# Performance work log

Hardware: AMD Instinct MI355X
Metric: run time of the kernel (lower is better)

Reference implementation:

```python
import jax, jax.numpy as jnp
import numpy as np

B, S, HID = 1, 2048, 4096
NH, NKV, D = 32, 8, 128          # query heads, kv heads, head_dim
GROUPS = NH // NKV               # GQA repeat factor = 4
WINDOW = 1024                    # sliding-window size
ROPE_BASE = 10000.0


def setup_inputs() -> dict:
    key = jax.random.key(0)
    k = jax.random.split(key, 5)
    hidden_states = jax.random.normal(k[0], (B, S, HID), jnp.float32)
    Wq = jax.random.normal(k[1], (HID, HID), jnp.float32) * 0.02
    Wk = jax.random.normal(k[2], (NKV * D, HID), jnp.float32) * 0.02
    Wv = jax.random.normal(k[3], (NKV * D, HID), jnp.float32) * 0.02
    Wo = jax.random.normal(k[4], (HID, HID), jnp.float32) * 0.02
    position_ids = jnp.arange(S, dtype=jnp.int64 if jax.config.jax_enable_x64 else jnp.int32)[None, :]
    # Sliding-window causal additive mask [B,1,S,S]: key j visible to query i iff i-WINDOW < j <= i
    i = jnp.arange(S)
    visible = (i[None, :] <= i[:, None]) & (i[:, None] - i[None, :] < WINDOW)
    neg = jnp.finfo(jnp.float32).min
    attention_mask = jnp.where(visible, 0.0, neg)[None, None, :, :].astype(jnp.float32)
    return {"hidden_states": hidden_states, "attention_mask": attention_mask,
            "position_ids": position_ids, "Wq": Wq, "Wk": Wk, "Wv": Wv, "Wo": Wo}


def _rotate_half(x):
    x1, x2 = x[..., : D // 2], x[..., D // 2:]
    return jnp.concatenate((-x2, x1), axis=-1)


def _rope_cos_sin(position_ids, dtype):
    # inv_freq over even dims; gather-by-position_ids == direct indexing
    inv_freq = 1.0 / (ROPE_BASE ** (jnp.arange(0, D, 2, dtype=jnp.float32) / D))  # [D/2]
    freqs = position_ids.astype(jnp.float32)[..., None] * inv_freq                # [B,S,D/2]
    emb = jnp.concatenate((freqs, freqs), axis=-1)                                # [B,S,D]
    cos = jnp.cos(emb)[:, None, :, :].astype(dtype)                               # [B,1,S,D]
    sin = jnp.sin(emb)[:, None, :, :].astype(dtype)
    return cos, sin


def reference(hidden_states, attention_mask, position_ids, Wq, Wk, Wv, Wo):
    bsz, q_len, _ = hidden_states.shape
    # projections (nn.Linear: y = x @ W.T)
    q = (hidden_states @ Wq.T).reshape(bsz, q_len, NH, D).transpose(0, 2, 1, 3)    # [B,NH,S,D]
    k = (hidden_states @ Wk.T).reshape(bsz, q_len, NKV, D).transpose(0, 2, 1, 3)   # [B,NKV,S,D]
    v = (hidden_states @ Wv.T).reshape(bsz, q_len, NKV, D).transpose(0, 2, 1, 3)
    cos, sin = _rope_cos_sin(position_ids, q.dtype)
    q = q * cos + _rotate_half(q) * sin
    k = k * cos + _rotate_half(k) * sin
    # GQA repeat_kv (repeat_interleave along head dim)
    k = jnp.repeat(k, GROUPS, axis=1)                                              # [B,NH,S,D]
    v = jnp.repeat(v, GROUPS, axis=1)
    scores = jnp.einsum('bhqd,bhkd->bhqk', q, k) / np.sqrt(D)                       # [B,NH,S,S]
    scores = scores + attention_mask
    scores = jnp.maximum(scores, jnp.finfo(scores.dtype).min)
    probs = jax.nn.softmax(scores.astype(jnp.float32), axis=-1).astype(q.dtype)
    out = jnp.einsum('bhqk,bhkd->bhqd', probs, v)                                   # [B,NH,S,D]
    out = out.transpose(0, 2, 1, 3).reshape(bsz, q_len, HID)
    return out @ Wo.T
```

## Files before the change

kernel.cpp:

```cpp
#include <hip/hip_runtime.h>

#define S_LEN 2048
#define HID   4096
#define NH    32
#define NKV   8
#define DH    128
#define KVD   (NKV*DH)
#define WIN   1024
#define NTOT  6144

typedef __bf16 bf16_t;
typedef __bf16 bfrag  __attribute__((ext_vector_type(8)));
typedef __bf16 bf4    __attribute__((ext_vector_type(4)));
typedef float  ffrag  __attribute__((ext_vector_type(4)));
typedef float  facc   __attribute__((ext_vector_type(16)));

__global__ __launch_bounds__(256) void f32_to_bf16_kernel(const float* __restrict__ src,
                                                          bf16_t* __restrict__ dst, int n4) {
  int i = blockIdx.x * 256 + threadIdx.x;
  if (i < n4) {
    ffrag v = *(const ffrag*)(src + (size_t)i * 4);
    bf4 o;
    o[0] = (bf16_t)v[0]; o[1] = (bf16_t)v[1]; o[2] = (bf16_t)v[2]; o[3] = (bf16_t)v[3];
    *(bf4*)(dst + (size_t)i * 4) = o;
  }
}

__global__ __launch_bounds__(256) void cvt4_kernel(const float* __restrict__ h,
    const float* __restrict__ Wq, const float* __restrict__ Wk, const float* __restrict__ Wv,
    bf16_t* __restrict__ hB, bf16_t* __restrict__ WqB,
    bf16_t* __restrict__ WkB, bf16_t* __restrict__ WvB) {
  int i = blockIdx.x * 256 + threadIdx.x;
  const int N0 = S_LEN * HID / 4;
  const int N1 = N0 + HID * HID / 4;
  const int N2 = N1 + KVD * HID / 4;
  const float* s; bf16_t* d; int off;
  if (i < N0)      { s = h;  d = hB;  off = i; }
  else if (i < N1) { s = Wq; d = WqB; off = i - N0; }
  else if (i < N2) { s = Wk; d = WkB; off = i - N1; }
  else             { s = Wv; d = WvB; off = i - N2; }
  ffrag v = *(const ffrag*)(s + (size_t)off * 4);
  bf4 o;
  o[0] = (bf16_t)v[0]; o[1] = (bf16_t)v[1]; o[2] = (bf16_t)v[2]; o[3] = (bf16_t)v[3];
  *(bf4*)(d + (size_t)off * 4) = o;
}


__device__ __forceinline__ void load_lds16(const bf16_t* g, bf16_t* l) {
  __builtin_amdgcn_global_load_lds((__attribute__((address_space(1))) void*)g,
                                   (__attribute__((address_space(3))) void*)l,
                                   16, 0, 0);
}

#define BARW() asm volatile("s_barrier" ::: "memory")
#define WAITV(n) asm volatile("s_waitcnt vmcnt(" #n ")" ::: "memory")
#define LGKM0() do { asm volatile("s_waitcnt lgkmcnt(0)" ::: "memory"); \
                     __builtin_amdgcn_sched_barrier(0); } while (0)

template <int BN, int OUT_MODE>
__device__ __forceinline__ void gemm_body(const bf16_t* __restrict__ A,
                                          const bf16_t* __restrict__ B,
                                          void* __restrict__ Cv,
                                          int row0, int col0,
                                          int N, bf16_t* lds) {
  constexpr int K     = 4096;
  constexpr int NT    = K / 64;
  constexpr int NB    = BN / 64;
  constexpr int WCOL  = BN / 2;
  constexpr int BSW   = BN / 32;
  constexpr int ABUFE = 128 * 64;
  constexpr int BBUFE = BN * 64;

  bf16_t* As0 = lds;
  bf16_t* Bs0 = lds + 2 * ABUFE;

  const int tid  = threadIdx.x;
  const int wave = tid >> 6;
  const int lane = tid & 63;
  const int wm = wave >> 1, wn = wave & 1;
  const int l31 = lane & 31, hi = lane >> 5, l7 = lane & 7;

  const int rsub = tid >> 3;
  const int sg   = (tid & 7) ^ (rsub & 7);
  const bf16_t* Ag = A + (size_t)(row0 + rsub) * K + sg * 8;
  const bf16_t* Bg = B + (size_t)(col0 + rsub) * K + sg * 8;
  const int wbase = wave * 512;

  int pgk[4];
#pragma unroll
  for (int ks = 0; ks < 4; ++ks) pgk[ks] = ((ks * 2 + hi) ^ l7) * 8;
  const int aoff = (wm * 64 + l31) * 64;
  const int boff = (wn * WCOL + l31) * 64;

  facc acc[2][NB];
#pragma unroll
  for (int mt = 0; mt < 2; ++mt)
#pragma unroll
    for (int nt = 0; nt < NB; ++nt)
#pragma unroll
      for (int j = 0; j < 16; ++j) acc[mt][nt][j] = 0.f;

  auto STAGE = [&](int t, int s) {
    const int ko = t * 64;
    bf16_t* as = As0 + s * ABUFE + wbase;
    bf16_t* bs = Bs0 + s * BBUFE + wbase;
#pragma unroll
    for (int i = 0; i < 4; ++i)
      load_lds16(Ag + (size_t)(i * 32) * K + ko, as + i * 2048);
#pragma unroll
    for (int i = 0; i < BSW; ++i)
      load_lds16(Bg + (size_t)(i * 32) * K + ko, bs + i * 2048);
  };

  STAGE(0, 0); STAGE(1, 1);
  if constexpr (BN == 192) { WAITV(10); } else { WAITV(8); }
  BARW();

  for (int t = 0; t < NT; ++t) {
    const int s = t & 1;
    const bf16_t* Asl = As0 + s * ABUFE;
    const bf16_t* Bsl = Bs0 + s * BBUFE;

#pragma unroll
    for (int ks = 0; ks < 4; ++ks) {
      bfrag av0 = *(const bfrag*)(Asl + aoff + pgk[ks]);
      bfrag av1 = *(const bfrag*)(Asl + aoff + 2048 + pgk[ks]);
      bfrag bv[NB];
#pragma unroll
      for (int nt = 0; nt < NB; ++nt)
        bv[nt] = *(const bfrag*)(Bsl + boff + nt * 2048 + pgk[ks]);
      __builtin_amdgcn_s_setprio(1);
#pragma unroll
      for (int nt = 0; nt < NB; ++nt)
        acc[0][nt] = __builtin_amdgcn_mfma_f32_32x32x16_bf16(av0, bv[nt], acc[0][nt], 0, 0, 0);
#pragma unroll
      for (int nt = 0; nt < NB; ++nt)
        acc[1][nt] = __builtin_amdgcn_mfma_f32_32x32x16_bf16(av1, bv[nt], acc[1][nt], 0, 0, 0);
      __builtin_amdgcn_s_setprio(0);
    }

    LGKM0();
    BARW();
    if (t + 2 < NT) STAGE(t + 2, s);
    if (t + 1 < NT) {
      if (t + 2 < NT) { if constexpr (BN == 192) { WAITV(10); } else { WAITV(8); } }
      else            { WAITV(0); }
      BARW();
    }
  }

  const int orow = row0 + wm * 64 + 4 * hi;
  const int ocol = col0 + wn * WCOL + l31;
#pragma unroll
  for (int mt = 0; mt < 2; ++mt)
#pragma unroll
    for (int nt = 0; nt < NB; ++nt)
#pragma unroll
      for (int j = 0; j < 16; ++j) {
        int r = orow + mt * 32 + (j & 3) + 8 * (j >> 2);
        size_t idx = (size_t)r * N + (ocol + nt * 32);
        if (OUT_MODE == 1) ((bf16_t*)Cv)[idx] = (bf16_t)acc[mt][nt][j];
        else               ((float*)Cv)[idx]  = acc[mt][nt][j];
      }
}

__global__ __launch_bounds__(256, 2) void gemm_qkv_kernel(const bf16_t* __restrict__ hB,
                                                          const bf16_t* __restrict__ Wqkv,
                                                          bf16_t* __restrict__ C) {
  __shared__ __align__(16) bf16_t lds[2 * 128 * 64 + 2 * 192 * 64];
  const int raw  = blockIdx.x;
  const int xcd  = raw & 7;
  const int slot = raw >> 3;
  const int bx   = xcd * 4 + (slot & 3);
  const int by   = slot >> 2;
  gemm_body<192, 1>(hB, Wqkv, C, by * 128, bx * 192, NTOT, lds);
}

__global__ __launch_bounds__(256, 2) void gemm_out_kernel(const bf16_t* __restrict__ A,
                                                          const bf16_t* __restrict__ B,
                                                          float* __restrict__ out) {
  __shared__ __align__(16) bf16_t lds[2 * 128 * 64 + 2 * 128 * 64];
  const int raw  = blockIdx.x;
  const int xcd  = raw & 7;
  const int slot = raw >> 3;
  const int bx   = xcd * 4 + (slot & 3);
  const int by   = slot >> 2;
  gemm_body<128, 0>(A, B, out, by * 128, bx * 128, HID, lds);
}

__global__ __launch_bounds__(256) void ropecvt_kernel(const bf16_t* __restrict__ Cqkv,
                                                      bf16_t* __restrict__ Qb,
                                                      bf16_t* __restrict__ Kb,
                                                      bf16_t* __restrict__ Vb) {
  int idx = blockIdx.x * 256 + threadIdx.x;
  int g  = idx & 7;
  int t  = idx >> 3;
  int hh = t % 48;
  int s  = t / 48;
  const bf16_t* r0 = Cqkv + (size_t)s * NTOT + hh * 128;
  bfrag a0 = *(const bfrag*)&r0[g * 8];
  bfrag a1 = *(const bfrag*)&r0[g * 8 + 64];
  bf16_t* p;
  bool rope;
  if (hh < NH)           { p = Qb + (size_t)s * HID + hh * DH;        rope = true; }
  else if (hh < NH+NKV)  { p = Kb + (size_t)s * KVD + (hh - NH) * DH; rope = true; }
  else                   { p = Vb + (size_t)s * KVD + (hh - 40) * DH; rope = false; }
  bfrag o1, o2;
#pragma unroll
  for (int j = 0; j < 8; ++j) {
    float x1 = (float)a0[j];
    float x2 = (float)a1[j];
    if (rope) {
      int d = g * 8 + j;
      float inv = exp2f((float)d * (-13.287712379549449f / 64.f));
      float ang = (float)s * inv;
      float sn = sinf(ang), cs = cosf(ang);
      o1[j] = (bf16_t)(x1 * cs - x2 * sn);
      o2[j] = (bf16_t)(x2 * cs + x1 * sn);
    } else {
      o1[j] = (bf16_t)x1;
      o2[j] = (bf16_t)x2;
    }
  }
  *(bfrag*)&p[g * 8]      = o1;
  *(bfrag*)&p[g * 8 + 64] = o2;
}

#define KS_STRIDE 136
#define VT_STRIDE 72
#define PS_STRIDE 72

__global__ __launch_bounds__(256, 3) void attn_kernel(const bf16_t* __restrict__ Q,
                                                      const bf16_t* __restrict__ Kc,
                                                      const bf16_t* __restrict__ Vc,
                                                      bf16_t* __restrict__ AO) {
  const int qt   = 31 - blockIdx.x;
  const int h    = blockIdx.y;
  const int kvh  = h >> 2;
  const int q0   = qt * 64;
  const int tid  = threadIdx.x;
  const int wq   = tid >> 6;
  const int lane = tid & 63;
  const int n    = lane & 15;
  const int quad = lane >> 4;
  const float scale = 0.08838834764831845f;

  __shared__ __align__(16) bf16_t Ks[64 * KS_STRIDE];
  __shared__ __align__(16) bf16_t VT[128 * VT_STRIDE];
  __shared__ __align__(16) bf16_t Ps[4][16 * PS_STRIDE];

  bfrag aq[4];
#pragma unroll
  for (int kc = 0; kc < 4; ++kc) {
    bfrag t = *(const bfrag*)&Q[(size_t)(q0 + wq * 16 + n) * HID + h * DH + kc * 32 + quad * 8];
#pragma unroll
    for (int e = 0; e < 8; ++e) t[e] = (bf16_t)((float)t[e] * scale);
    aq[kc] = t;
  }

  ffrag acc[8];
#pragma unroll
  for (int dt = 0; dt < 8; ++dt) { acc[dt][0] = 0.f; acc[dt][1] = 0.f; acc[dt][2] = 0.f; acc[dt][3] = 0.f; }
  float lrow[4] = {0.f, 0.f, 0.f, 0.f};

  const int ktlo = (q0 >= WIN) ? ((q0 - (WIN - 1)) >> 6) : 0;
  const int kthi = (q0 + 63) >> 6;

  const int kg = tid & 15;
  const int dg = tid >> 4;

  bfrag pk[4], pv[4];
  {
    const int k0 = ktlo * 64;
#pragma unroll
    for (int i = 0; i < 4; ++i) {
      int pos = i * 256 + tid;
      pk[i] = *(const bfrag*)&Kc[(size_t)(k0 + (pos >> 4)) * KVD + kvh * DH + (pos & 15) * 8];
    }
#pragma unroll
    for (int j = 0; j < 4; ++j)
      pv[j] = *(const bfrag*)&Vc[(size_t)(k0 + j * 16 + kg) * KVD + kvh * DH + dg * 8];
  }

  for (int kt = ktlo; kt <= kthi; ++kt) {
    const int k0 = kt * 64;
    __syncthreads();
#pragma unroll
    for (int i = 0; i < 4; ++i) {
      int pos = i * 256 + tid;
      *(bfrag*)&Ks[(pos >> 4) * KS_STRIDE + (pos & 15) * 8] = pk[i];
    }
#pragma unroll
    for (int i = 0; i < 8; ++i) {
      bf4 pkk;
      pkk[0] = pv[0][i]; pkk[1] = pv[1][i]; pkk[2] = pv[2][i]; pkk[3] = pv[3][i];
      *(bf4*)&VT[(dg * 8 + i) * VT_STRIDE + kg * 4] = pkk;
    }
    __syncthreads();
    if (kt < kthi) {
      const int k1 = k0 + 64;
#pragma unroll
      for (int i = 0; i < 4; ++i) {
        int pos = i * 256 + tid;
        pk[i] = *(const bfrag*)&Kc[(size_t)(k1 + (pos >> 4)) * KVD + kvh * DH + (pos & 15) * 8];
      }
#pragma unroll
      for (int j = 0; j < 4; ++j)
        pv[j] = *(const bfrag*)&Vc[(size_t)(k1 + j * 16 + kg) * KVD + kvh * DH + dg * 8];
    }

    ffrag s[4];
#pragma unroll
    for (int nt = 0; nt < 4; ++nt) { s[nt][0] = 0.f; s[nt][1] = 0.f; s[nt][2] = 0.f; s[nt][3] = 0.f; }
#pragma unroll
    for (int kc = 0; kc < 4; ++kc) {
      bfrag bk[4];
#pragma unroll
      for (int nt = 0; nt < 4; ++nt)
        bk[nt] = *(const bfrag*)&Ks[(nt * 16 + n) * KS_STRIDE + kc * 32 + quad * 8];
      __builtin_amdgcn_s_setprio(1);
#pragma unroll
      for (int nt = 0; nt < 4; ++nt)
        s[nt] = __builtin_amdgcn_mfma_f32_16x16x32_bf16(aq[kc], bk[nt], s[nt], 0, 0, 0);
      __builtin_amdgcn_s_setprio(0);
    }

    const bool full = (k0 + 63 <= q0) && (q0 + 63 - k0 < WIN);
    if (!full) {
#pragma unroll
      for (int nt = 0; nt < 4; ++nt)
#pragma unroll
        for (int r = 0; r < 4; ++r) {
          int q = q0 + wq * 16 + quad * 4 + r;
          int k = k0 + nt * 16 + n;
          bool vis = (k <= q) && ((q - k) < WIN);
          if (!vis) s[nt][r] = -1e30f;
        }
    }

#pragma unroll
    for (int r = 0; r < 4; ++r) {
      bf4 pkk;
      float ps0 = __expf(s[0][r]);
      float ps1 = __expf(s[1][r]);
      float ps2 = __expf(s[2][r]);
      float ps3 = __expf(s[3][r]);
      lrow[r] += (ps0 + ps1) + (ps2 + ps3);
      pkk[0] = (bf16_t)ps0; pkk[1] = (bf16_t)ps1; pkk[2] = (bf16_t)ps2; pkk[3] = (bf16_t)ps3;
      *(bf4*)&Ps[wq][(quad * 4 + r) * PS_STRIDE + n * 4] = pkk;
    }

#pragma unroll
    for (int kc = 0; kc < 2; ++kc) {
      bfrag ap = *(const bfrag*)&Ps[wq][n * PS_STRIDE + kc * 32 + quad * 8];
#pragma unroll
      for (int dt = 0; dt < 8; dt += 4) {
        bfrag bv0 = *(const bfrag*)&VT[((dt + 0) * 16 + n) * VT_STRIDE + kc * 32 + quad * 8];
        bfrag bv1 = *(const bfrag*)&VT[((dt + 1) * 16 + n) * VT_STRIDE + kc * 32 + quad * 8];
        bfrag bv2 = *(const bfrag*)&VT[((dt + 2) * 16 + n) * VT_STRIDE + kc * 32 + quad * 8];
        bfrag bv3 = *(const bfrag*)&VT[((dt + 3) * 16 + n) * VT_STRIDE + kc * 32 + quad * 8];
        __builtin_amdgcn_s_setprio(1);
        acc[dt + 0] = __builtin_amdgcn_mfma_f32_16x16x32_bf16(ap, bv0, acc[dt + 0], 0, 0, 0);
        acc[dt + 1] = __builtin_amdgcn_mfma_f32_16x16x32_bf16(ap, bv1, acc[dt + 1], 0, 0, 0);
        acc[dt + 2] = __builtin_amdgcn_mfma_f32_16x16x32_bf16(ap, bv2, acc[dt + 2], 0, 0, 0);
        acc[dt + 3] = __builtin_amdgcn_mfma_f32_16x16x32_bf16(ap, bv3, acc[dt + 3], 0, 0, 0);
        __builtin_amdgcn_s_setprio(0);
      }
    }
  }

#pragma unroll
  for (int off = 1; off < 16; off <<= 1)
#pragma unroll
    for (int r = 0; r < 4; ++r) lrow[r] += __shfl_xor(lrow[r], off);
  float inv[4];
#pragma unroll
  for (int r = 0; r < 4; ++r) inv[r] = 1.f / lrow[r];
#pragma unroll
  for (int dt = 0; dt < 8; ++dt)
#pragma unroll
    for (int r = 0; r < 4; ++r)
      AO[(size_t)(q0 + wq * 16 + quad * 4 + r) * HID + h * DH + dt * 16 + n] =
          (bf16_t)(acc[dt][r] * inv[r]);
}

extern "C" void kernel_launch(void* const* d_in, const int* in_sizes, int n_in,
                              void* d_out, int out_size, void* d_ws, size_t ws_size,
                              hipStream_t stream) {
  const float* h  = (const float*)d_in[0];
  const float* Wq = (const float*)d_in[3];
  const float* Wk = (const float*)d_in[4];
  const float* Wv = (const float*)d_in[5];
  const float* Wo = (const float*)d_in[6];
  float* out = (float*)d_out;

  char* ws = (char*)d_ws;
  const size_t MB = (size_t)1 << 20;
  bf16_t* hB    = (bf16_t*)(ws + 0 * MB);
  bf16_t* Qb    = (bf16_t*)(ws + 0 * MB);
  bf16_t* WqB   = (bf16_t*)(ws + 16 * MB);
  bf16_t* WkB   = (bf16_t*)(ws + 48 * MB);
  bf16_t* WvB   = (bf16_t*)(ws + 56 * MB);
  bf16_t* Cqkv  = (bf16_t*)(ws + 64 * MB);
  bf16_t* WoB   = (bf16_t*)(ws + 64 * MB);
  bf16_t* AOb   = (bf16_t*)(ws + 96 * MB);
  bf16_t* Kb    = (bf16_t*)(ws + 112 * MB);
  bf16_t* Vb    = (bf16_t*)(ws + 116 * MB);

  cvt4_kernel<<<(S_LEN * HID + HID * HID + 2 * KVD * HID) / 4 / 256, 256, 0, stream>>>(
      h, Wq, Wk, Wv, hB, WqB, WkB, WvB);

  gemm_qkv_kernel<<<512, 256, 0, stream>>>(hB, WqB, Cqkv);

  ropecvt_kernel<<<(S_LEN * 48 * 8) / 256, 256, 0, stream>>>(Cqkv, Qb, Kb, Vb);

  f32_to_bf16_kernel<<<(HID * HID / 4 + 255) / 256, 256, 0, stream>>>(Wo, WoB, HID * HID / 4);

  attn_kernel<<<dim3(32, NH), 256, 0, stream>>>(Qb, Kb, Vb, AOb);

  gemm_out_kernel<<<512, 256, 0, stream>>>(AOb, WoB, out);
}
```

Baseline: 458.5 us.

## Use 512-thread 16x16x32 MFMA GEMM for QKV and precompute RoPE table

```diff
diff --git a/kernel.cpp b/kernel.cpp
--- a/kernel.cpp
+++ b/kernel.cpp
@@ -45,6 +45,13 @@
   *(bf4*)(d + (size_t)off * 4) = o;
 }
 
+__global__ __launch_bounds__(256) void rope_table_kernel(float2* __restrict__ tab) {
+  int i = blockIdx.x * 256 + threadIdx.x;
+  int s = i >> 6, d = i & 63;
+  float inv = exp2f((float)d * (-13.287712379549449f / 64.f));
+  float ang = (float)s * inv;
+  tab[i] = make_float2(cosf(ang), sinf(ang));
+}
 
 __device__ __forceinline__ void load_lds16(const bf16_t* g, bf16_t* l) {
   __builtin_amdgcn_global_load_lds((__attribute__((address_space(1))) void*)g,
@@ -57,12 +64,136 @@
 #define LGKM0() do { asm volatile("s_waitcnt lgkmcnt(0)" ::: "memory"); \
                      __builtin_amdgcn_sched_barrier(0); } while (0)
 
+template <int BNR, int OUT_MODE>
+__device__ __forceinline__ void gemm16_body(const bf16_t* __restrict__ A,
+                                            const bf16_t* __restrict__ B,
+                                            void* __restrict__ Cv,
+                                            int N, bf16_t* lds) {
+  constexpr int K     = 4096;
+  constexpr int NT    = K / 64;
+  constexpr int NTF   = BNR / 64;
+  constexpr int WC    = BNR / 4;
+  constexpr int ABUFE = 128 * 64;
+  constexpr int BBUFE = BNR * 64;
+
+  bf16_t* As0 = lds;
+  bf16_t* Bs0 = lds + 2 * ABUFE;
+
+  const int raw  = blockIdx.x;
+  const int xcd  = raw & 7;
+  const int slot = raw >> 3;
+  const int bx   = xcd * 4 + (slot & 3);
+  const int by   = slot >> 2;
+  const int row0 = by * 128;
+  const int col0 = bx * BNR;
+
+  const int tid  = threadIdx.x;
+  const int wave = tid >> 6;
+  const int lane = tid & 63;
+  const int wr = wave >> 2, wc = wave & 3;
+  const int n = lane & 15, qd = lane >> 4;
+
+  const int rsub = tid >> 3;
+  const int sg   = (tid & 7) ^ (rsub & 7);
+  const bf16_t* Ag = A + (size_t)(row0 + rsub) * K + sg * 8;
+  const bf16_t* Bg = B + (size_t)(col0 + rsub) * K + sg * 8;
+  const int wbase = wave * 512;
+
+  const int pg0 = ( qd      ^ (n & 7)) * 8;
+  const int pg1 = ((4 | qd) ^ (n & 7)) * 8;
+  const int abase = (wr * 64 + n) * 64;
+  const int bbase = (wc * WC + n) * 64;
+
+  ffrag acc[4][NTF];
+#pragma unroll
+  for (int mt = 0; mt < 4; ++mt)
+#pragma unroll
+    for (int nt = 0; nt < NTF; ++nt) {
+      acc[mt][nt][0] = 0.f; acc[mt][nt][1] = 0.f; acc[mt][nt][2] = 0.f; acc[mt][nt][3] = 0.f;
+    }
+
+  auto STAGE = [&](int t, int s) {
+    const int ko = t * 64;
+    bf16_t* as = As0 + s * ABUFE + wbase;
+    bf16_t* bs = Bs0 + s * BBUFE + wbase;
+    load_lds16(Ag + ko, as);
+    load_lds16(Ag + (size_t)64 * K + ko, as + 4096);
+    load_lds16(Bg + ko, bs);
+    load_lds16(Bg + (size_t)64 * K + ko, bs + 4096);
+    if constexpr (BNR == 192) load_lds16(Bg + (size_t)128 * K + ko, bs + 8192);
+  };
+
+  STAGE(0, 0); STAGE(1, 1);
+  if constexpr (BNR == 192) { WAITV(5); } else { WAITV(4); }
+  BARW();
+
+  for (int t = 0; t < NT; ++t) {
+    const int s = t & 1;
+    const bf16_t* Asl = As0 + s * ABUFE;
+    const bf16_t* Bsl = Bs0 + s * BBUFE;
+    bfrag av[4], bv[NTF];
+
+#pragma unroll
+    for (int mt = 0; mt < 4; ++mt) av[mt] = *(const bfrag*)(Asl + abase + mt * 1024 + pg0);
+#pragma unroll
+    for (int nt = 0; nt < NTF; ++nt) bv[nt] = *(const bfrag*)(Bsl + bbase + nt * 1024 + pg0);
+    __builtin_amdgcn_s_setprio(1);
+#pragma unroll
+    for (int mt = 0; mt < 4; ++mt)
+#pragma unroll
+      for (int nt = 0; nt < NTF; ++nt)
+        acc[mt][nt] = __builtin_amdgcn_mfma_f32_16x16x32_bf16(av[mt], bv[nt], acc[mt][nt], 0, 0, 0);
+    __builtin_amdgcn_s_setprio(0);
+
+#pragma unroll
+    for (int mt = 0; mt < 4; ++mt) av[mt] = *(const bfrag*)(Asl + abase + mt * 1024 + pg1);
+#pragma unroll
+    for (int nt = 0; nt < NTF; ++nt) bv[nt] = *(const bfrag*)(Bsl + bbase + nt * 1024 + pg1);
+    __builtin_amdgcn_s_setprio(1);
+#pragma unroll
+    for (int mt = 0; mt < 4; ++mt)
+#pragma unroll
+      for (int nt = 0; nt < NTF; ++nt)
+        acc[mt][nt] = __builtin_amdgcn_mfma_f32_16x16x32_bf16(av[mt], bv[nt], acc[mt][nt], 0, 0, 0);
+    __builtin_amdgcn_s_setprio(0);
+
+    LGKM0();
+    BARW();
+    if (t + 2 < NT) STAGE(t + 2, s);
+    if (t + 1 < NT) {
+      if (t + 2 < NT) { if constexpr (BNR == 192) { WAITV(5); } else { WAITV(4); } }
+      else            { WAITV(0); }
+      BARW();
+    }
+  }
+
+  const int orow = row0 + wr * 64 + qd * 4;
+  const int ocol = col0 + wc * WC + n;
+#pragma unroll
+  for (int mt = 0; mt < 4; ++mt)
+#pragma unroll
+    for (int nt = 0; nt < NTF; ++nt)
+#pragma unroll
+      for (int r = 0; r < 4; ++r) {
+        size_t idx = (size_t)(orow + mt * 16 + r) * N + (ocol + nt * 16);
+        if (OUT_MODE == 1) ((bf16_t*)Cv)[idx] = (bf16_t)acc[mt][nt][r];
+        else               ((float*)Cv)[idx]  = acc[mt][nt][r];
+      }
+}
+
+__global__ __launch_bounds__(512, 4) void gemm_qkv_kernel(const bf16_t* __restrict__ hB,
+                                                          const bf16_t* __restrict__ Wqkv,
+                                                          bf16_t* __restrict__ C) {
+  __shared__ __align__(16) bf16_t lds[2 * 128 * 64 + 2 * 192 * 64];
+  gemm16_body<192, 1>(hB, Wqkv, C, NTOT, lds);
+}
+
 template <int BN, int OUT_MODE>
-__device__ __forceinline__ void gemm_body(const bf16_t* __restrict__ A,
-                                          const bf16_t* __restrict__ B,
-                                          void* __restrict__ Cv,
-                                          int row0, int col0,
-                                          int N, bf16_t* lds) {
+__device__ __forceinline__ void gemm32_body(const bf16_t* __restrict__ A,
+                                            const bf16_t* __restrict__ B,
+                                            void* __restrict__ Cv,
+                                            int row0, int col0,
+                                            int N, bf16_t* lds) {
   constexpr int K     = 4096;
   constexpr int NT    = K / 64;
   constexpr int NB    = BN / 64;
@@ -113,7 +244,7 @@
   };
 
   STAGE(0, 0); STAGE(1, 1);
-  if constexpr (BN == 192) { WAITV(10); } else { WAITV(8); }
+  WAITV(8);
   BARW();
 
   for (int t = 0; t < NT; ++t) {
@@ -143,7 +274,7 @@
     BARW();
     if (t + 2 < NT) STAGE(t + 2, s);
     if (t + 1 < NT) {
-      if (t + 2 < NT) { if constexpr (BN == 192) { WAITV(10); } else { WAITV(8); } }
+      if (t + 2 < NT) { WAITV(8); }
       else            { WAITV(0); }
       BARW();
     }
@@ -162,18 +293,6 @@
         if (OUT_MODE == 1) ((bf16_t*)Cv)[idx] = (bf16_t)acc[mt][nt][j];
         else               ((float*)Cv)[idx]  = acc[mt][nt][j];
       }
-}
-
-__global__ __launch_bounds__(256, 2) void gemm_qkv_kernel(const bf16_t* __restrict__ hB,
-                                                          const bf16_t* __restrict__ Wqkv,
-                                                          bf16_t* __restrict__ C) {
-  __shared__ __align__(16) bf16_t lds[2 * 128 * 64 + 2 * 192 * 64];
-  const int raw  = blockIdx.x;
-  const int xcd  = raw & 7;
-  const int slot = raw >> 3;
-  const int bx   = xcd * 4 + (slot & 3);
-  const int by   = slot >> 2;
-  gemm_body<192, 1>(hB, Wqkv, C, by * 128, bx * 192, NTOT, lds);
 }
 
 __global__ __launch_bounds__(256, 2) void gemm_out_kernel(const bf16_t* __restrict__ A,
@@ -185,10 +304,11 @@
   const int slot = raw >> 3;
   const int bx   = xcd * 4 + (slot & 3);
   const int by   = slot >> 2;
-  gemm_body<128, 0>(A, B, out, by * 128, bx * 128, HID, lds);
+  gemm32_body<128, 0>(A, B, out, by * 128, bx * 128, HID, lds);
 }
 
 __global__ __launch_bounds__(256) void ropecvt_kernel(const bf16_t* __restrict__ Cqkv,
+                                                      const float2* __restrict__ tab,
                                                       bf16_t* __restrict__ Qb,
                                                       bf16_t* __restrict__ Kb,
                                                       bf16_t* __restrict__ Vb) {
@@ -206,21 +326,19 @@
   else if (hh < NH+NKV)  { p = Kb + (size_t)s * KVD + (hh - NH) * DH; rope = true; }
   else                   { p = Vb + (size_t)s * KVD + (hh - 40) * DH; rope = false; }
   bfrag o1, o2;
-#pragma unroll
-  for (int j = 0; j < 8; ++j) {
-    float x1 = (float)a0[j];
-    float x2 = (float)a1[j];
-    if (rope) {
-      int d = g * 8 + j;
-      float inv = exp2f((float)d * (-13.287712379549449f / 64.f));
-      float ang = (float)s * inv;
-      float sn = sinf(ang), cs = cosf(ang);
-      o1[j] = (bf16_t)(x1 * cs - x2 * sn);
-      o2[j] = (bf16_t)(x2 * cs + x1 * sn);
-    } else {
-      o1[j] = (bf16_t)x1;
-      o2[j] = (bf16_t)x2;
-    }
+  if (rope) {
+    const float2* tb = tab + s * 64 + g * 8;
+#pragma unroll
+    for (int j = 0; j < 8; ++j) {
+      float x1 = (float)a0[j];
+      float x2 = (float)a1[j];
+      float2 cs = tb[j];
+      o1[j] = (bf16_t)(x1 * cs.x - x2 * cs.y);
+      o2[j] = (bf16_t)(x2 * cs.x + x1 * cs.y);
+    }
+  } else {
+#pragma unroll
+    for (int j = 0; j < 8; ++j) { o1[j] = a0[j]; o2[j] = a1[j]; }
   }
   *(bfrag*)&p[g * 8]      = o1;
   *(bfrag*)&p[g * 8 + 64] = o2;
@@ -402,17 +520,20 @@
   bf16_t* WkB   = (bf16_t*)(ws + 48 * MB);
   bf16_t* WvB   = (bf16_t*)(ws + 56 * MB);
   bf16_t* Cqkv  = (bf16_t*)(ws + 64 * MB);
+  float2* Rtab  = (float2*)(ws + 88 * MB);
   bf16_t* WoB   = (bf16_t*)(ws + 64 * MB);
   bf16_t* AOb   = (bf16_t*)(ws + 96 * MB);
   bf16_t* Kb    = (bf16_t*)(ws + 112 * MB);
   bf16_t* Vb    = (bf16_t*)(ws + 116 * MB);
 
+  rope_table_kernel<<<(S_LEN * 64) / 256, 256, 0, stream>>>(Rtab);
+
   cvt4_kernel<<<(S_LEN * HID + HID * HID + 2 * KVD * HID) / 4 / 256, 256, 0, stream>>>(
       h, Wq, Wk, Wv, hB, WqB, WkB, WvB);
 
-  gemm_qkv_kernel<<<512, 256, 0, stream>>>(hB, WqB, Cqkv);
-
-  ropecvt_kernel<<<(S_LEN * 48 * 8) / 256, 256, 0, stream>>>(Cqkv, Qb, Kb, Vb);
+  gemm_qkv_kernel<<<512, 512, 0, stream>>>(hB, WqB, Cqkv);
+
+  ropecvt_kernel<<<(S_LEN * 48 * 8) / 256, 256, 0, stream>>>(Cqkv, Rtab, Qb, Kb, Vb);
 
   f32_to_bf16_kernel<<<(HID * HID / 4 + 255) / 256, 256, 0, stream>>>(Wo, WoB, HID * HID / 4);
 
```

Result: no change. 452.7 us (-1.3%).
